# Optimization experiments

Measured on AMD Instinct MI355X. Metric: run time of the kernel, lower is better.

## Reference

```python
import jax, jax.numpy as jnp
import numpy as np

B, S, H, E, D, K = 2, 2048, 2048, 8, 2048, 2


def setup_inputs() -> dict:
    key = jax.random.key(0)
    ks = jax.random.split(key, 4)
    # lecun_normal-style scaling: std = 1/sqrt(fan_in)
    return {
        "x": jax.random.normal(ks[0], (B, S, H), jnp.float32),
        "router_w": jax.random.normal(ks[1], (H, E), jnp.float32) / np.sqrt(H).astype(np.float32),
        "router_b": jnp.zeros((E,), jnp.float32),
        "expert_w": jax.random.normal(ks[2], (E, H, D), jnp.float32) / np.sqrt(H).astype(np.float32),
        "expert_b": jnp.zeros((E, D), jnp.float32),
        "out_w": jax.random.normal(ks[3], (D, D), jnp.float32) / np.sqrt(D).astype(np.float32),
        "out_b": jnp.zeros((D,), jnp.float32),
    }


def reference(x, router_w, router_b, expert_w, expert_b, out_w, out_b):
    num_experts = expert_w.shape[0]
    # Router: logits -> softmax -> top-2 -> renormalize
    router_logits = jnp.einsum("bsh,he->bse", x, router_w) + router_b
    router_probs = jax.nn.softmax(router_logits, axis=-1)
    top_k_probs, top_k_indices = jax.lax.top_k(router_probs, K)  # [B,S,K]
    top_k_probs = top_k_probs / jnp.sum(top_k_probs, axis=-1, keepdims=True)
    # Per-expert gate weight: sum of top-k probs routed to that expert. [B,S,E]
    onehot = jax.nn.one_hot(top_k_indices, num_experts, dtype=x.dtype)  # [B,S,K,E]
    gates = jnp.einsum("bsk,bske->bse", top_k_probs, onehot)
    # Dense per-expert GEMM + gelu (mask-and-multiply MoE; gate==0 kills unrouted tokens)
    expert_out = jax.nn.gelu(jnp.einsum("bsh,ehd->ebsd", x, expert_w) + expert_b[:, None, None, :])
    combined = jnp.einsum("bse,ebsd->bsd", gates, expert_out)
    # Output projection
    return jnp.einsum("bsd,df->bsf", combined, out_w) + out_b
```

## Files before the change

### kernel.cpp

```cpp
#include <hip/hip_runtime.h>
#include <stdint.h>

#define H_DIM 2048
#define E_NUM 8
#define D_DIM 2048
#define NTOK 4096
#define BM 128
#define BN 128
#define BK 32

typedef __bf16 bf16x8 __attribute__((ext_vector_type(8)));
typedef float f32x4 __attribute__((ext_vector_type(4)));

__device__ __forceinline__ unsigned short f2bf(float f) {
    union { float f; uint32_t u; } c; c.f = f;
    uint32_t r = (c.u + 0x7FFFu + ((c.u >> 16) & 1u)) >> 16;
    return (unsigned short)r;
}
__device__ __forceinline__ float bf2f(unsigned short h) {
    union { float f; uint32_t u; } c; c.u = ((uint32_t)h) << 16;
    return c.f;
}

__device__ __forceinline__ void gl_lds16(const unsigned short* g, unsigned short* l) {
    __builtin_amdgcn_global_load_lds(
        (const __attribute__((address_space(1))) unsigned int*)g,
        (__attribute__((address_space(3))) unsigned int*)l, 16, 0, 0);
}

__global__ __launch_bounds__(256) void router_cvt_kernel(
    const float* __restrict__ x, const float* __restrict__ rw,
    const float* __restrict__ rb, int* __restrict__ counts,
    uint32_t* __restrict__ tok, float* __restrict__ gate,
    unsigned short* __restrict__ xb) {
    int t = (blockIdx.x * 256 + threadIdx.x) >> 6;
    int lane = threadIdx.x & 63;
    const float* xr = x + (size_t)t * H_DIM;
    unsigned short* xo = xb + (size_t)t * H_DIM;
    float p[E_NUM];
#pragma unroll
    for (int e = 0; e < E_NUM; e++) p[e] = 0.f;
#pragma unroll
    for (int pass = 0; pass < H_DIM / 256; pass++) {
        int h = pass * 256 + lane * 4;
        float4 v = *(const float4*)(xr + h);
        ushort4 o;
        o.x = f2bf(v.x); o.y = f2bf(v.y); o.z = f2bf(v.z); o.w = f2bf(v.w);
        *(ushort4*)(xo + h) = o;
        const float* r0 = rw + (size_t)h * E_NUM;
#pragma unroll
        for (int e = 0; e < E_NUM; e++)
            p[e] += v.x * r0[e] + v.y * r0[e + 8] + v.z * r0[e + 16] + v.w * r0[e + 24];
    }
#pragma unroll
    for (int e = 0; e < E_NUM; e++) {
#pragma unroll
        for (int off = 1; off < 64; off <<= 1) p[e] += __shfl_xor(p[e], off, 64);
    }
    if (lane == 0) {
        float l[E_NUM];
#pragma unroll
        for (int e = 0; e < E_NUM; e++) l[e] = p[e] + rb[e];
        int e0 = 0;
#pragma unroll
        for (int e = 1; e < E_NUM; e++) if (l[e] > l[e0]) e0 = e;
        int e1 = (e0 == 0) ? 1 : 0;
#pragma unroll
        for (int e = 0; e < E_NUM; e++) if (e != e0 && l[e] > l[e1]) e1 = e;
        float g0 = 1.f / (1.f + __expf(l[e1] - l[e0]));
        float g1 = 1.f - g0;
        int p0 = atomicAdd(&counts[e0], 1);
        tok[e0 * NTOK + p0] = (uint32_t)t;
        gate[e0 * NTOK + p0] = g0;
        int p1 = atomicAdd(&counts[e1], 1);
        tok[e1 * NTOK + p1] = (uint32_t)t | (1u << 16);
        gate[e1 * NTOK + p1] = g1;
    }
}

__global__ __launch_bounds__(256) void transpose_cvt_kernel(
    const float* __restrict__ src, unsigned short* __restrict__ dst,
    int K_, int N_) {
    __shared__ unsigned short tile[64][72];
    size_t moff = (size_t)blockIdx.z * (size_t)K_ * N_;
    const float* s = src + moff;
    unsigned short* d = dst + moff;
    int k0 = blockIdx.y * 64, n0 = blockIdx.x * 64;
    int r = threadIdx.x >> 4;
    int c = (threadIdx.x & 15) * 4;
#pragma unroll
    for (int p = 0; p < 4; p++) {
        int k = p * 16 + r;
        float4 v = *(const float4*)(s + (size_t)(k0 + k) * N_ + n0 + c);
        tile[k][c + 0] = f2bf(v.x);
        tile[k][c + 1] = f2bf(v.y);
        tile[k][c + 2] = f2bf(v.z);
        tile[k][c + 3] = f2bf(v.w);
    }
    __syncthreads();
#pragma unroll
    for (int p = 0; p < 4; p++) {
        int n = p * 16 + r;
        ushort4 o;
        o.x = tile[c + 0][n];
        o.y = tile[c + 1][n];
        o.z = tile[c + 2][n];
        o.w = tile[c + 3][n];
        *(ushort4*)(d + (size_t)(n0 + n) * K_ + k0 + c) = o;
    }
}

__global__ __launch_bounds__(256) void expert_gemm_kernel(
    const unsigned short* __restrict__ xb,
    const unsigned short* __restrict__ ewT,
    const float* __restrict__ eb,
    const int* __restrict__ counts,
    const uint32_t* __restrict__ tok,
    const float* __restrict__ gate,
    unsigned short* __restrict__ Y)
{
    int e = blockIdx.z;
    int cnt = counts[e];
    int m0 = blockIdx.y * BM;
    if (m0 >= cnt) return;
    int n0 = blockIdx.x * BN;

    __shared__ unsigned short As[BM][BK];
    __shared__ unsigned short Bs[BN][BK];
    __shared__ uint32_t tok_s[BM];
    __shared__ float gate_s[BM];

    int tid = threadIdx.x;
    if (tid < BM) {
        int idx = m0 + tid;
        uint32_t tk = 0; float g = 0.f;
        if (idx < cnt) { tk = tok[e * NTOK + idx]; g = gate[e * NTOK + idx]; }
        tok_s[tid] = tk; gate_s[tid] = g;
    }
    __syncthreads();

    int lane = tid & 63;
    int wave = tid >> 6;
    int sr = lane >> 2;
    int sc = (lane & 3) * 8;
    int r0 = wave * 32 + sr;
    int r1 = wave * 32 + 16 + sr;
    const unsigned short* agp0 = xb + (size_t)(tok_s[r0] & 0xFFFFu) * H_DIM + sc;
    const unsigned short* agp1 = xb + (size_t)(tok_s[r1] & 0xFFFFu) * H_DIM + sc;
    const unsigned short* bbase = ewT + (size_t)e * D_DIM * H_DIM;
    const unsigned short* bgp0 = bbase + (size_t)(n0 + r0) * H_DIM + sc;
    const unsigned short* bgp1 = bbase + (size_t)(n0 + r1) * H_DIM + sc;
    unsigned short* la0 = &As[wave * 32][0];
    unsigned short* la1 = &As[wave * 32 + 16][0];
    unsigned short* lb0 = &Bs[wave * 32][0];
    unsigned short* lb1 = &Bs[wave * 32 + 16][0];

    int wm = (wave >> 1) * 64;
    int wn = (wave & 1) * 64;
    int row16 = lane & 15;
    int quad = lane >> 4;
    int k8 = quad * 8;

    f32x4 acc[4][4];
#pragma unroll
    for (int i = 0; i < 4; i++)
#pragma unroll
        for (int j = 0; j < 4; j++) acc[i][j] = (f32x4)(0.f);

    for (int kk = 0; kk < H_DIM; kk += BK) {
        __syncthreads();
        gl_lds16(agp0 + kk, la0);
        gl_lds16(agp1 + kk, la1);
        gl_lds16(bgp0 + kk, lb0);
        gl_lds16(bgp1 + kk, lb1);
        __syncthreads();
        bf16x8 af[4], bff[4];
#pragma unroll
        for (int i = 0; i < 4; i++)
            af[i] = *(const bf16x8*)&As[wm + i * 16 + row16][k8];
#pragma unroll
        for (int j = 0; j < 4; j++)
            bff[j] = *(const bf16x8*)&Bs[wn + j * 16 + row16][k8];
#pragma unroll
        for (int i = 0; i < 4; i++)
#pragma unroll
            for (int j = 0; j < 4; j++)
                acc[i][j] = __builtin_amdgcn_mfma_f32_16x16x32_bf16(
                    af[i], bff[j], acc[i][j], 0, 0, 0);
    }

#pragma unroll
    for (int i = 0; i < 4; i++) {
        int rbase = wm + i * 16 + quad * 4;
#pragma unroll
        for (int j = 0; j < 4; j++) {
            int n = n0 + wn + j * 16 + row16;
            float bias = eb[e * D_DIM + n];
#pragma unroll
            for (int r = 0; r < 4; r++) {
                int lrow = rbase + r;
                if (m0 + lrow < cnt) {
                    uint32_t tk = tok_s[lrow];
                    float g = gate_s[lrow];
                    float v = acc[i][j][r] + bias;
                    float q = 0.7978845608028654f * (v + 0.044715f * v * v * v);
                    float gl = v / (1.f + __expf(-2.f * q));
                    int token = tk & 0xFFFF;
                    int slot = (tk >> 16) & 1;
                    Y[((size_t)token * 2 + slot) * D_DIM + n] = f2bf(g * gl);
                }
            }
        }
    }
}

__global__ __launch_bounds__(256) void combine_kernel(
    const unsigned short* __restrict__ Y, unsigned short* __restrict__ comb) {
    int i = blockIdx.x * 256 + threadIdx.x;
    int t = i >> 8;
    int dc = (i & 255) * 8;
    uint4 u0 = *(const uint4*)(Y + (size_t)t * 2 * D_DIM + dc);
    uint4 u1 = *(const uint4*)(Y + ((size_t)t * 2 + 1) * D_DIM + dc);
    uint4 o;
    uint32_t* po = (uint32_t*)&o;
    const uint32_t* p0 = (const uint32_t*)&u0;
    const uint32_t* p1 = (const uint32_t*)&u1;
#pragma unroll
    for (int k = 0; k < 4; k++) {
        uint32_t a = p0[k], b = p1[k];
        float s0 = bf2f((unsigned short)(a & 0xFFFF)) + bf2f((unsigned short)(b & 0xFFFF));
        float s1 = bf2f((unsigned short)(a >> 16)) + bf2f((unsigned short)(b >> 16));
        po[k] = (uint32_t)f2bf(s0) | ((uint32_t)f2bf(s1) << 16);
    }
    *(uint4*)(comb + (size_t)t * D_DIM + dc) = o;
}

__global__ __launch_bounds__(256) void out_gemm_kernel(
    const unsigned short* __restrict__ comb,
    const unsigned short* __restrict__ owT,
    const float* __restrict__ ob,
    float* __restrict__ out) {
    int m0 = blockIdx.y * BM, n0 = blockIdx.x * BN;
    __shared__ unsigned short As[BM][BK];
    __shared__ unsigned short Bs[BN][BK];
    int tid = threadIdx.x;
    int lane = tid & 63;
    int wave = tid >> 6;
    int sr = lane >> 2;
    int sc = (lane & 3) * 8;
    int r0 = wave * 32 + sr;
    int r1 = wave * 32 + 16 + sr;
    const unsigned short* agp0 = comb + (size_t)(m0 + r0) * D_DIM + sc;
    const unsigned short* agp1 = comb + (size_t)(m0 + r1) * D_DIM + sc;
    const unsigned short* bgp0 = owT + (size_t)(n0 + r0) * D_DIM + sc;
    const unsigned short* bgp1 = owT + (size_t)(n0 + r1) * D_DIM + sc;
    unsigned short* la0 = &As[wave * 32][0];
    unsigned short* la1 = &As[wave * 32 + 16][0];
    unsigned short* lb0 = &Bs[wave * 32][0];
    unsigned short* lb1 = &Bs[wave * 32 + 16][0];

    int wm = (wave >> 1) * 64;
    int wn = (wave & 1) * 64;
    int row16 = lane & 15;
    int quad = lane >> 4;
    int k8 = quad * 8;

    f32x4 acc[4][4];
#pragma unroll
    for (int i = 0; i < 4; i++)
#pragma unroll
        for (int j = 0; j < 4; j++) acc[i][j] = (f32x4)(0.f);

    for (int kk = 0; kk < D_DIM; kk += BK) {
        __syncthreads();
        gl_lds16(agp0 + kk, la0);
        gl_lds16(agp1 + kk, la1);
        gl_lds16(bgp0 + kk, lb0);
        gl_lds16(bgp1 + kk, lb1);
        __syncthreads();
        bf16x8 af[4], bff[4];
#pragma unroll
        for (int i = 0; i < 4; i++)
            af[i] = *(const bf16x8*)&As[wm + i * 16 + row16][k8];
#pragma unroll
        for (int j = 0; j < 4; j++)
            bff[j] = *(const bf16x8*)&Bs[wn + j * 16 + row16][k8];
#pragma unroll
        for (int i = 0; i < 4; i++)
#pragma unroll
            for (int j = 0; j < 4; j++)
                acc[i][j] = __builtin_amdgcn_mfma_f32_16x16x32_bf16(
                    af[i], bff[j], acc[i][j], 0, 0, 0);
    }

#pragma unroll
    for (int i = 0; i < 4; i++) {
        int rbase = m0 + wm + i * 16 + quad * 4;
#pragma unroll
        for (int j = 0; j < 4; j++) {
            int n = n0 + wn + j * 16 + row16;
            float bias = ob[n];
#pragma unroll
            for (int r = 0; r < 4; r++) {
                out[(size_t)(rbase + r) * D_DIM + n] = acc[i][j][r] + bias;
            }
        }
    }
}

extern "C" void kernel_launch(void* const* d_in, const int* in_sizes, int n_in,
                              void* d_out, int out_size, void* d_ws, size_t ws_size,
                              hipStream_t stream) {
    const float* x        = (const float*)d_in[0];
    const float* router_w = (const float*)d_in[1];
    const float* router_b = (const float*)d_in[2];
    const float* expert_w = (const float*)d_in[3];
    const float* expert_b = (const float*)d_in[4];
    const float* out_w    = (const float*)d_in[5];
    const float* out_b    = (const float*)d_in[6];
    float* out = (float*)d_out;

    char* w = (char*)d_ws;
    int* counts = (int*)w;
    uint32_t* tok = (uint32_t*)(w + 256);
    float* gate = (float*)(w + 256 + E_NUM * NTOK * 4);
    size_t off = 256 + (size_t)2 * E_NUM * NTOK * 4;
    unsigned short* xb = (unsigned short*)(w + off);
    off += (size_t)NTOK * H_DIM * 2;
    unsigned short* ewT = (unsigned short*)(w + off);
    off += (size_t)E_NUM * H_DIM * D_DIM * 2;
    unsigned short* owT = (unsigned short*)(w + off);
    off += (size_t)D_DIM * D_DIM * 2;
    unsigned short* Y = (unsigned short*)(w + off);
    off += (size_t)NTOK * 2 * D_DIM * 2;
    unsigned short* comb = (unsigned short*)(w + off);

    hipMemsetAsync(d_ws, 0, 256, stream);
    router_cvt_kernel<<<NTOK / 4, 256, 0, stream>>>(x, router_w, router_b,
                                                    counts, tok, gate, xb);
    transpose_cvt_kernel<<<dim3(32, 32, 8), 256, 0, stream>>>(expert_w, ewT, H_DIM, D_DIM);
    transpose_cvt_kernel<<<dim3(32, 32, 1), 256, 0, stream>>>(out_w, owT, D_DIM, D_DIM);
    expert_gemm_kernel<<<dim3(16, 32, 8), 256, 0, stream>>>(xb, ewT, expert_b, counts, tok, gate, Y);
    combine_kernel<<<NTOK * D_DIM / 8 / 256, 256, 0, stream>>>(Y, comb);
    out_gemm_kernel<<<dim3(16, 32), 256, 0, stream>>>(comb, owT, out_b, out);
}
```

Before: 534.7 us.

## Double BK with XOR-swizzled LDS, compact expert tile table, wider transpose stores

```diff
diff --git a/kernel.cpp b/kernel.cpp
--- a/kernel.cpp
+++ b/kernel.cpp
@@ -7,7 +7,8 @@
 #define NTOK 4096
 #define BM 128
 #define BN 128
-#define BK 32
+#define BK 64
+#define MAXTILES 71
 
 typedef __bf16 bf16x8 __attribute__((ext_vector_type(8)));
 typedef float f32x4 __attribute__((ext_vector_type(4)));
@@ -78,35 +79,46 @@
     }
 }
 
+__global__ void build_tiles_kernel(const int* __restrict__ counts,
+                                   int* __restrict__ ntiles,
+                                   int2* __restrict__ tab) {
+    if (threadIdx.x == 0 && blockIdx.x == 0) {
+        int off = 0;
+        for (int e = 0; e < E_NUM; e++) {
+            int c = counts[e];
+            for (int m0 = 0; m0 < c; m0 += BM) tab[off++] = make_int2(e, m0);
+        }
+        *ntiles = off;
+    }
+}
+
 __global__ __launch_bounds__(256) void transpose_cvt_kernel(
     const float* __restrict__ src, unsigned short* __restrict__ dst,
     int K_, int N_) {
-    __shared__ unsigned short tile[64][72];
+    __shared__ unsigned short t[64][136];
     size_t moff = (size_t)blockIdx.z * (size_t)K_ * N_;
     const float* s = src + moff;
     unsigned short* d = dst + moff;
-    int k0 = blockIdx.y * 64, n0 = blockIdx.x * 64;
-    int r = threadIdx.x >> 4;
-    int c = (threadIdx.x & 15) * 4;
+    int n0 = blockIdx.x * 64, k0 = blockIdx.y * 128;
+    int tid = threadIdx.x;
+    int rr = tid >> 4;
+    int c4 = (tid & 15) * 4;
+#pragma unroll
+    for (int p = 0; p < 8; p++) {
+        int k = p * 16 + rr;
+        float4 v = *(const float4*)(s + (size_t)(k0 + k) * N_ + n0 + c4);
+        t[c4 + 0][k] = f2bf(v.x);
+        t[c4 + 1][k] = f2bf(v.y);
+        t[c4 + 2][k] = f2bf(v.z);
+        t[c4 + 3][k] = f2bf(v.w);
+    }
+    __syncthreads();
+    int kc = (tid & 15) * 8;
 #pragma unroll
     for (int p = 0; p < 4; p++) {
-        int k = p * 16 + r;
-        float4 v = *(const float4*)(s + (size_t)(k0 + k) * N_ + n0 + c);
-        tile[k][c + 0] = f2bf(v.x);
-        tile[k][c + 1] = f2bf(v.y);
-        tile[k][c + 2] = f2bf(v.z);
-        tile[k][c + 3] = f2bf(v.w);
-    }
-    __syncthreads();
-#pragma unroll
-    for (int p = 0; p < 4; p++) {
-        int n = p * 16 + r;
-        ushort4 o;
-        o.x = tile[c + 0][n];
-        o.y = tile[c + 1][n];
-        o.z = tile[c + 2][n];
-        o.w = tile[c + 3][n];
-        *(ushort4*)(d + (size_t)(n0 + n) * K_ + k0 + c) = o;
+        int n = p * 16 + rr;
+        uint4 v = *(const uint4*)&t[n][kc];
+        *(uint4*)(d + (size_t)(n0 + n) * K_ + k0 + kc) = v;
     }
 }
 
@@ -115,14 +127,16 @@
     const unsigned short* __restrict__ ewT,
     const float* __restrict__ eb,
     const int* __restrict__ counts,
+    const int* __restrict__ ntiles,
+    const int2* __restrict__ tab,
     const uint32_t* __restrict__ tok,
     const float* __restrict__ gate,
     unsigned short* __restrict__ Y)
 {
-    int e = blockIdx.z;
+    if ((int)blockIdx.y >= *ntiles) return;
+    int2 te = tab[blockIdx.y];
+    int e = te.x, m0 = te.y;
     int cnt = counts[e];
-    int m0 = blockIdx.y * BM;
-    if (m0 >= cnt) return;
     int n0 = blockIdx.x * BN;
 
     __shared__ unsigned short As[BM][BK];
@@ -141,25 +155,36 @@
 
     int lane = tid & 63;
     int wave = tid >> 6;
-    int sr = lane >> 2;
-    int sc = (lane & 3) * 8;
-    int r0 = wave * 32 + sr;
-    int r1 = wave * 32 + 16 + sr;
-    const unsigned short* agp0 = xb + (size_t)(tok_s[r0] & 0xFFFFu) * H_DIM + sc;
-    const unsigned short* agp1 = xb + (size_t)(tok_s[r1] & 0xFFFFu) * H_DIM + sc;
+    int srow = lane >> 3;
+    int scol = ((lane & 7) ^ srow) * 8;
     const unsigned short* bbase = ewT + (size_t)e * D_DIM * H_DIM;
-    const unsigned short* bgp0 = bbase + (size_t)(n0 + r0) * H_DIM + sc;
-    const unsigned short* bgp1 = bbase + (size_t)(n0 + r1) * H_DIM + sc;
-    unsigned short* la0 = &As[wave * 32][0];
-    unsigned short* la1 = &As[wave * 32 + 16][0];
-    unsigned short* lb0 = &Bs[wave * 32][0];
-    unsigned short* lb1 = &Bs[wave * 32 + 16][0];
+    const unsigned short* aptr[4];
+    const unsigned short* bptr[4];
+    unsigned short* lA[4];
+    unsigned short* lB[4];
+#pragma unroll
+    for (int u = 0; u < 4; u++) {
+        int r = wave * 32 + u * 8 + srow;
+        aptr[u] = xb + (size_t)(tok_s[r] & 0xFFFFu) * H_DIM + scol;
+        bptr[u] = bbase + (size_t)(n0 + r) * H_DIM + scol;
+        lA[u] = &As[wave * 32 + u * 8][0];
+        lB[u] = &Bs[wave * 32 + u * 8][0];
+    }
 
     int wm = (wave >> 1) * 64;
     int wn = (wave & 1) * 64;
     int row16 = lane & 15;
     int quad = lane >> 4;
-    int k8 = quad * 8;
+    int aoffA[4], aoffB[4];
+#pragma unroll
+    for (int i = 0; i < 4; i++) {
+        int ra = wm + i * 16 + row16;
+        aoffA[i] = ra * (BK * 2) + ((quad ^ (ra & 7)) * 16);
+        int rb = wn + i * 16 + row16;
+        aoffB[i] = rb * (BK * 2) + ((quad ^ (rb & 7)) * 16);
+    }
+    const char* pA = (const char*)&As[0][0];
+    const char* pB = (const char*)&Bs[0][0];
 
     f32x4 acc[4][4];
 #pragma unroll
@@ -169,24 +194,31 @@
 
     for (int kk = 0; kk < H_DIM; kk += BK) {
         __syncthreads();
-        gl_lds16(agp0 + kk, la0);
-        gl_lds16(agp1 + kk, la1);
-        gl_lds16(bgp0 + kk, lb0);
-        gl_lds16(bgp1 + kk, lb1);
+#pragma unroll
+        for (int u = 0; u < 4; u++) gl_lds16(aptr[u] + kk, lA[u]);
+#pragma unroll
+        for (int u = 0; u < 4; u++) gl_lds16(bptr[u] + kk, lB[u]);
         __syncthreads();
-        bf16x8 af[4], bff[4];
-#pragma unroll
-        for (int i = 0; i < 4; i++)
-            af[i] = *(const bf16x8*)&As[wm + i * 16 + row16][k8];
-#pragma unroll
-        for (int j = 0; j < 4; j++)
-            bff[j] = *(const bf16x8*)&Bs[wn + j * 16 + row16][k8];
+        bf16x8 a0[4], b0[4], a1[4], b1[4];
+#pragma unroll
+        for (int i = 0; i < 4; i++) {
+            a0[i] = *(const bf16x8*)(pA + aoffA[i]);
+            b0[i] = *(const bf16x8*)(pB + aoffB[i]);
+            a1[i] = *(const bf16x8*)(pA + (aoffA[i] ^ 64));
+            b1[i] = *(const bf16x8*)(pB + (aoffB[i] ^ 64));
+        }
 #pragma unroll
         for (int i = 0; i < 4; i++)
 #pragma unroll
             for (int j = 0; j < 4; j++)
                 acc[i][j] = __builtin_amdgcn_mfma_f32_16x16x32_bf16(
-                    af[i], bff[j], acc[i][j], 0, 0, 0);
+                    a0[i], b0[j], acc[i][j], 0, 0, 0);
+#pragma unroll
+        for (int i = 0; i < 4; i++)
+#pragma unroll
+            for (int j = 0; j < 4; j++)
+                acc[i][j] = __builtin_amdgcn_mfma_f32_16x16x32_bf16(
+                    a1[i], b1[j], acc[i][j], 0, 0, 0);
     }
 
 #pragma unroll
@@ -246,24 +278,35 @@
     int tid = threadIdx.x;
     int lane = tid & 63;
     int wave = tid >> 6;
-    int sr = lane >> 2;
-    int sc = (lane & 3) * 8;
-    int r0 = wave * 32 + sr;
-    int r1 = wave * 32 + 16 + sr;
-    const unsigned short* agp0 = comb + (size_t)(m0 + r0) * D_DIM + sc;
-    const unsigned short* agp1 = comb + (size_t)(m0 + r1) * D_DIM + sc;
-    const unsigned short* bgp0 = owT + (size_t)(n0 + r0) * D_DIM + sc;
-    const unsigned short* bgp1 = owT + (size_t)(n0 + r1) * D_DIM + sc;
-    unsigned short* la0 = &As[wave * 32][0];
-    unsigned short* la1 = &As[wave * 32 + 16][0];
-    unsigned short* lb0 = &Bs[wave * 32][0];
-    unsigned short* lb1 = &Bs[wave * 32 + 16][0];
+    int srow = lane >> 3;
+    int scol = ((lane & 7) ^ srow) * 8;
+    const unsigned short* aptr[4];
+    const unsigned short* bptr[4];
+    unsigned short* lA[4];
+    unsigned short* lB[4];
+#pragma unroll
+    for (int u = 0; u < 4; u++) {
+        int r = wave * 32 + u * 8 + srow;
+        aptr[u] = comb + (size_t)(m0 + r) * D_DIM + scol;
+        bptr[u] = owT + (size_t)(n0 + r) * D_DIM + scol;
+        lA[u] = &As[wave * 32 + u * 8][0];
+        lB[u] = &Bs[wave * 32 + u * 8][0];
+    }
 
     int wm = (wave >> 1) * 64;
     int wn = (wave & 1) * 64;
     int row16 = lane & 15;
     int quad = lane >> 4;
-    int k8 = quad * 8;
+    int aoffA[4], aoffB[4];
+#pragma unroll
+    for (int i = 0; i < 4; i++) {
+        int ra = wm + i * 16 + row16;
+        aoffA[i] = ra * (BK * 2) + ((quad ^ (ra & 7)) * 16);
+        int rb = wn + i * 16 + row16;
+        aoffB[i] = rb * (BK * 2) + ((quad ^ (rb & 7)) * 16);
+    }
+    const char* pA = (const char*)&As[0][0];
+    const char* pB = (const char*)&Bs[0][0];
 
     f32x4 acc[4][4];
 #pragma unroll
@@ -273,24 +316,31 @@
 
     for (int kk = 0; kk < D_DIM; kk += BK) {
         __syncthreads();
-        gl_lds16(agp0 + kk, la0);
-        gl_lds16(agp1 + kk, la1);
-        gl_lds16(bgp0 + kk, lb0);
-        gl_lds16(bgp1 + kk, lb1);
+#pragma unroll
+        for (int u = 0; u < 4; u++) gl_lds16(aptr[u] + kk, lA[u]);
+#pragma unroll
+        for (int u = 0; u < 4; u++) gl_lds16(bptr[u] + kk, lB[u]);
         __syncthreads();
-        bf16x8 af[4], bff[4];
-#pragma unroll
-        for (int i = 0; i < 4; i++)
-            af[i] = *(const bf16x8*)&As[wm + i * 16 + row16][k8];
-#pragma unroll
-        for (int j = 0; j < 4; j++)
-            bff[j] = *(const bf16x8*)&Bs[wn + j * 16 + row16][k8];
+        bf16x8 a0[4], b0[4], a1[4], b1[4];
+#pragma unroll
+        for (int i = 0; i < 4; i++) {
+            a0[i] = *(const bf16x8*)(pA + aoffA[i]);
+            b0[i] = *(const bf16x8*)(pB + aoffB[i]);
+            a1[i] = *(const bf16x8*)(pA + (aoffA[i] ^ 64));
+            b1[i] = *(const bf16x8*)(pB + (aoffB[i] ^ 64));
+        }
 #pragma unroll
         for (int i = 0; i < 4; i++)
 #pragma unroll
             for (int j = 0; j < 4; j++)
                 acc[i][j] = __builtin_amdgcn_mfma_f32_16x16x32_bf16(
-                    af[i], bff[j], acc[i][j], 0, 0, 0);
+                    a0[i], b0[j], acc[i][j], 0, 0, 0);
+#pragma unroll
+        for (int i = 0; i < 4; i++)
+#pragma unroll
+            for (int j = 0; j < 4; j++)
+                acc[i][j] = __builtin_amdgcn_mfma_f32_16x16x32_bf16(
+                    a1[i], b1[j], acc[i][j], 0, 0, 0);
     }
 
 #pragma unroll
@@ -322,9 +372,11 @@
 
     char* w = (char*)d_ws;
     int* counts = (int*)w;
-    uint32_t* tok = (uint32_t*)(w + 256);
-    float* gate = (float*)(w + 256 + E_NUM * NTOK * 4);
-    size_t off = 256 + (size_t)2 * E_NUM * NTOK * 4;
+    int* ntiles = (int*)(w + 64);
+    int2* tab = (int2*)(w + 128);
+    uint32_t* tok = (uint32_t*)(w + 1024);
+    float* gate = (float*)(w + 1024 + E_NUM * NTOK * 4);
+    size_t off = 1024 + (size_t)2 * E_NUM * NTOK * 4;
     unsigned short* xb = (unsigned short*)(w + off);
     off += (size_t)NTOK * H_DIM * 2;
     unsigned short* ewT = (unsigned short*)(w + off);
@@ -335,12 +387,14 @@
     off += (size_t)NTOK * 2 * D_DIM * 2;
     unsigned short* comb = (unsigned short*)(w + off);
 
-    hipMemsetAsync(d_ws, 0, 256, stream);
+    hipMemsetAsync(d_ws, 0, 1024, stream);
     router_cvt_kernel<<<NTOK / 4, 256, 0, stream>>>(x, router_w, router_b,
                                                     counts, tok, gate, xb);
-    transpose_cvt_kernel<<<dim3(32, 32, 8), 256, 0, stream>>>(expert_w, ewT, H_DIM, D_DIM);
-    transpose_cvt_kernel<<<dim3(32, 32, 1), 256, 0, stream>>>(out_w, owT, D_DIM, D_DIM);
-    expert_gemm_kernel<<<dim3(16, 32, 8), 256, 0, stream>>>(xb, ewT, expert_b, counts, tok, gate, Y);
+    build_tiles_kernel<<<1, 64, 0, stream>>>(counts, ntiles, tab);
+    transpose_cvt_kernel<<<dim3(32, 16, 8), 256, 0, stream>>>(expert_w, ewT, H_DIM, D_DIM);
+    transpose_cvt_kernel<<<dim3(32, 16, 1), 256, 0, stream>>>(out_w, owT, D_DIM, D_DIM);
+    expert_gemm_kernel<<<dim3(16, MAXTILES), 256, 0, stream>>>(
+        xb, ewT, expert_b, counts, ntiles, tab, tok, gate, Y);
     combine_kernel<<<NTOK * D_DIM / 8 / 256, 256, 0, stream>>>(Y, comb);
     out_gemm_kernel<<<dim3(16, 32), 256, 0, stream>>>(comb, owT, out_b, out);
 }
```

After: 543.5 us. No clear change (+1.7%).
